# Optimization experiments

Hardware: AMD Instinct MI355X
Metric: run time of the kernel (lower is better)

## Reference

```python
import jax, jax.numpy as jnp
import numpy as np

B, T, IN, H = 64, 128, 1024, 2048  # batch, seq_len, input_size, hidden_size


def setup_inputs() -> dict:
    key = jax.random.key(0)
    k_x, k_wx, k_wa, k_b = jax.random.split(key, 4)
    x = jax.random.normal(k_x, (B, T, IN), dtype=jnp.float32)
    # stacked gate weights in torch LSTM order [i, f, g, o]; scaled like trained weights
    Wx = jax.random.normal(k_wx, (4 * H, IN), dtype=jnp.float32) * 0.05
    Wa = jax.random.normal(k_wa, (4 * H, H), dtype=jnp.float32) * 0.05
    b = jax.random.normal(k_b, (4 * H,), dtype=jnp.float32) * 0.05
    a0 = jnp.zeros((B, H), dtype=jnp.float32)
    c0 = jnp.zeros((B, H), dtype=jnp.float32)
    return {"x": x, "Wx": Wx, "Wa": Wa, "b": b, "a0": a0, "c0": c0}


def reference(x, Wx, Wa, b, a0, c0):
    # LSTM interval-propagation forward pass (the concrete forward of My_lstm):
    #   y* = W*x @ x_t + b* + W*a @ a_{t-1}
    #   c_t = sigmoid(yf) * c_{t-1} + sigmoid(yi) * tanh(yg)
    #   a_t = sigmoid(yo) * tanh(c_t)
    # a0=c0=0 reproduces the a0=None/c0=None code path exactly.
    H_ = Wa.shape[1]

    def step(carry, x_t):
        a_prev, c_prev = carry  # each [B, H]
        # one fused GEMM over all 4 gates: [B, 4H]
        y = x_t @ Wx.T + a_prev @ Wa.T + b
        yi, yf, yg, yo = jnp.split(y, 4, axis=-1)
        c_t = jax.nn.sigmoid(yf) * c_prev + jax.nn.sigmoid(yi) * jnp.tanh(yg)
        a_t = jax.nn.sigmoid(yo) * jnp.tanh(c_t)
        return (a_t, c_t), (a_t, c_t, yi, yf, yg, yo)

    xs = jnp.swapaxes(x, 0, 1)  # [T, B, IN] for scan over time
    _, (a, c, yi, yf, yg, yo) = jax.lax.scan(step, (a0, c0), xs)
    # back to [B, T, H] as in the torch module
    to_bt = lambda z: jnp.swapaxes(z, 0, 1)
    return (to_bt(a), to_bt(c), to_bt(yi), to_bt(yf), to_bt(yg), to_bt(yo))
```

## Files before the change

### kernel.cpp

```cpp
#include <hip/hip_runtime.h>
#include <hip/hip_bf16.h>

#define B_   64
#define T_   128
#define IN_  1024
#define H_   2048
#define H4_  8192
#define BT_  8192
#define BTH_ 16777216LL

typedef __attribute__((ext_vector_type(8))) short short8;
typedef __attribute__((ext_vector_type(4))) float f32x4;

__device__ __forceinline__ unsigned short f32_to_bf16_rne(float f) {
    union { float f; unsigned int u; } v; v.f = f;
    return (unsigned short)((v.u + 0x7fffu + ((v.u >> 16) & 1u)) >> 16);
}

__device__ __forceinline__ void gload_lds16(const unsigned short* g, unsigned short* l) {
    __builtin_amdgcn_global_load_lds(
        (const __attribute__((address_space(1))) unsigned int*)g,
        (__attribute__((address_space(3))) unsigned int*)l,
        16, 0, 0);
}

__global__ void cvt_bf16_kernel(const float* __restrict__ src,
                                unsigned short* __restrict__ dst, long n) {
    long i = ((long)blockIdx.x * blockDim.x + threadIdx.x) * 4;
    long stride = (long)gridDim.x * blockDim.x * 4;
    for (; i < n; i += stride) {
        float4 v = *reinterpret_cast<const float4*>(src + i);
        ushort4 o;
        o.x = f32_to_bf16_rne(v.x);
        o.y = f32_to_bf16_rne(v.y);
        o.z = f32_to_bf16_rne(v.z);
        o.w = f32_to_bf16_rne(v.w);
        *reinterpret_cast<ushort4*>(dst + i) = o;
    }
}

__global__ void copy_f32_kernel(const float* __restrict__ src,
                                float* __restrict__ dst, long n) {
    long i = ((long)blockIdx.x * blockDim.x + threadIdx.x) * 4;
    long stride = (long)gridDim.x * blockDim.x * 4;
    for (; i < n; i += stride)
        *reinterpret_cast<float4*>(dst + i) =
            *reinterpret_cast<const float4*>(src + i);
}

__global__ __launch_bounds__(256) void gemm_yx(
    const unsigned short* __restrict__ Xb,
    const unsigned short* __restrict__ Wxb,
    const float* __restrict__ bias,
    float* __restrict__ out)
{
    int bid = blockIdx.x;
    int sw  = (bid & 7) * 512 + (bid >> 3);
    int nb  = sw & 63;
    int mb  = sw >> 6;
    int m0  = mb * 128;
    int n0  = nb * 128;

    int tid  = threadIdx.x;
    int wave = tid >> 6;
    int lane = tid & 63;
    int col  = lane & 15;
    int quad = lane >> 4;
    int wm   = wave >> 1;
    int wn   = wave & 1;

    __shared__ unsigned short As[128 * 32];
    __shared__ unsigned short Bs[128 * 32];

    f32x4 acc[4][4];
#pragma unroll
    for (int i = 0; i < 4; i++)
#pragma unroll
        for (int j = 0; j < 4; j++) acc[i][j] = (f32x4){0.f, 0.f, 0.f, 0.f};

    for (int k0 = 0; k0 < IN_; k0 += 32) {
#pragma unroll
        for (int r = 0; r < 2; r++) {
            int idx = r * 256 + tid;
            int row = idx >> 2;
            int c8  = (idx & 3) * 8;
            int dbase = (r * 256 + wave * 64) * 8;
            gload_lds16(Xb  + (size_t)(m0 + row) * IN_ + k0 + c8, &As[dbase]);
            gload_lds16(Wxb + (size_t)(n0 + row) * IN_ + k0 + c8, &Bs[dbase]);
        }
        __syncthreads();

        short8 af[4], bf[4];
#pragma unroll
        for (int mt = 0; mt < 4; mt++)
            af[mt] = *(const short8*)&As[(wm * 64 + mt * 16 + col) * 32 + quad * 8];
#pragma unroll
        for (int nt = 0; nt < 4; nt++)
            bf[nt] = *(const short8*)&Bs[(wn * 64 + nt * 16 + col) * 32 + quad * 8];
#pragma unroll
        for (int mt = 0; mt < 4; mt++)
#pragma unroll
            for (int nt = 0; nt < 4; nt++)
                acc[mt][nt] = __builtin_amdgcn_mfma_f32_16x16x32_bf16(
                    af[mt], bf[nt], acc[mt][nt], 0, 0, 0);
        __syncthreads();
    }

#pragma unroll
    for (int nt = 0; nt < 4; nt++) {
        int n = n0 + wn * 64 + nt * 16 + col;
        int g = n >> 11;
        int h = n & 2047;
        float bv = bias[n];
        float* slab = out + (size_t)(2 + g) * BTH_ + h;
#pragma unroll
        for (int mt = 0; mt < 4; mt++)
#pragma unroll
            for (int r = 0; r < 4; r++) {
                int m = m0 + wm * 64 + mt * 16 + quad * 4 + r;
                slab[(size_t)m * H_] = acc[mt][nt][r] + bv;
            }
    }
}

__global__ __launch_bounds__(512) void lstm_step(
    const unsigned short* __restrict__ Wab,
    const unsigned short* __restrict__ a_prev,
    float* __restrict__ c_state,
    unsigned short* __restrict__ a_next,
    float* __restrict__ out,
    int t)
{
    int j    = blockIdx.x;
    int mh   = j & 1;
    int ht   = j >> 1;
    int h0   = ht * 16;
    int m0   = mh * 32;
    int w    = threadIdx.x >> 6;
    int g    = w & 3;
    int kh   = w >> 2;
    int lane = threadIdx.x & 63;
    int col  = lane & 15;
    int quad = lane >> 4;

    const unsigned short* brow =
        Wab + (size_t)(g * H_ + h0 + col) * H_ + kh * 1024;
    const unsigned short* arow0 =
        a_prev + (size_t)(m0 + col) * H_ + kh * 1024;
    const unsigned short* arow1 =
        a_prev + (size_t)(m0 + 16 + col) * H_ + kh * 1024;

    f32x4 acc[2];
    acc[0] = (f32x4){0.f, 0.f, 0.f, 0.f};
    acc[1] = acc[0];

#pragma unroll 4
    for (int k0 = 0; k0 < 1024; k0 += 32) {
        short8 bfrag = *(const short8*)(brow  + k0 + quad * 8);
        short8 af0   = *(const short8*)(arow0 + k0 + quad * 8);
        short8 af1   = *(const short8*)(arow1 + k0 + quad * 8);
        acc[0] = __builtin_amdgcn_mfma_f32_16x16x32_bf16(af0, bfrag, acc[0], 0, 0, 0);
        acc[1] = __builtin_amdgcn_mfma_f32_16x16x32_bf16(af1, bfrag, acc[1], 0, 0, 0);
    }

    __shared__ float yt[2][4][32][17];
#pragma unroll
    for (int mt = 0; mt < 2; mt++)
#pragma unroll
        for (int r = 0; r < 4; r++) {
            int lm = mt * 16 + quad * 4 + r;
            yt[kh][g][lm][col] = acc[mt][r];
        }
    __syncthreads();

    int f  = threadIdx.x;
    int lm = f >> 4;
    int hl = f & 15;
    int b  = m0 + lm;
    int h  = h0 + hl;
    long long oidx = ((long long)b * T_ + t) * H_ + h;

    float yi = yt[0][0][lm][hl] + yt[1][0][lm][hl] + out[2 * BTH_ + oidx];
    float yf = yt[0][1][lm][hl] + yt[1][1][lm][hl] + out[3 * BTH_ + oidx];
    float yg = yt[0][2][lm][hl] + yt[1][2][lm][hl] + out[4 * BTH_ + oidx];
    float yo = yt[0][3][lm][hl] + yt[1][3][lm][hl] + out[5 * BTH_ + oidx];
    out[2 * BTH_ + oidx] = yi;
    out[3 * BTH_ + oidx] = yf;
    out[4 * BTH_ + oidx] = yg;
    out[5 * BTH_ + oidx] = yo;

    float cp = c_state[b * H_ + h];
    float si = 1.f / (1.f + __expf(-yi));
    float sf = 1.f / (1.f + __expf(-yf));
    float so = 1.f / (1.f + __expf(-yo));
    float tg = tanhf(yg);
    float ct = sf * cp + si * tg;
    float at = so * tanhf(ct);

    c_state[b * H_ + h] = ct;
    out[oidx]          = at;
    out[BTH_ + oidx]   = ct;
    a_next[b * H_ + h] = f32_to_bf16_rne(at);
}

extern "C" void kernel_launch(void* const* d_in, const int* in_sizes, int n_in,
                              void* d_out, int out_size, void* d_ws, size_t ws_size,
                              hipStream_t stream) {
    const float* x    = (const float*)d_in[0];
    const float* Wx   = (const float*)d_in[1];
    const float* Wa   = (const float*)d_in[2];
    const float* bias = (const float*)d_in[3];
    const float* a0   = (const float*)d_in[4];
    const float* c0   = (const float*)d_in[5];
    float* out = (float*)d_out;

    unsigned short* xb    = (unsigned short*)d_ws;
    unsigned short* wxb   = xb  + (size_t)BT_ * IN_;
    unsigned short* wab   = wxb + (size_t)H4_ * IN_;
    unsigned short* abuf0 = wab + (size_t)H4_ * H_;
    unsigned short* abuf1 = abuf0 + (size_t)B_ * H_;
    float*          cst   = (float*)(abuf1 + (size_t)B_ * H_);

    cvt_bf16_kernel<<<2048, 256, 0, stream>>>(x,  xb,  (long)BT_ * IN_);
    cvt_bf16_kernel<<<2048, 256, 0, stream>>>(Wx, wxb, (long)H4_ * IN_);
    cvt_bf16_kernel<<<2048, 256, 0, stream>>>(Wa, wab, (long)H4_ * H_);
    cvt_bf16_kernel<<<128,  256, 0, stream>>>(a0, abuf0, (long)B_ * H_);
    copy_f32_kernel<<<128,  256, 0, stream>>>(c0, cst,   (long)B_ * H_);

    gemm_yx<<<(BT_ / 128) * (H4_ / 128), 256, 0, stream>>>(xb, wxb, bias, out);

    for (int t = 0; t < T_; ++t) {
        const unsigned short* ap = (t & 1) ? abuf1 : abuf0;
        unsigned short*       an = (t & 1) ? abuf0 : abuf1;
        lstm_step<<<256, 512, 0, stream>>>(wab, ap, cst, an, out, t);
    }
}
```

Baseline: 3.964 ms.

## Replace per-timestep LSTM launches with persistent cooperative kernel holding weights in registers

The 128 per-timestep kernel launches are replaced by a single cooperative persistent kernel. It loads each block's slice of the recurrent weights into registers once, keeps the cell state in a register, and separates timesteps with grid.sync. This removes per-step launch overhead and the repeated weight reloads from global memory, at the cost of heavy register pressure and a grid-wide barrier every step. The input-projection GEMM also gains an XOR swizzle on its LDS layout to reduce bank conflicts.

Measured after the change: 15.44 ms. 3.9x slower.

```diff
diff --git a/kernel.cpp b/kernel.cpp
--- a/kernel.cpp
+++ b/kernel.cpp
@@ -1,5 +1,8 @@
 #include <hip/hip_runtime.h>
 #include <hip/hip_bf16.h>
+#include <hip/hip_cooperative_groups.h>
+
+namespace cg = cooperative_groups;
 
 #define B_   64
 #define T_   128
@@ -39,15 +42,6 @@
     }
 }
 
-__global__ void copy_f32_kernel(const float* __restrict__ src,
-                                float* __restrict__ dst, long n) {
-    long i = ((long)blockIdx.x * blockDim.x + threadIdx.x) * 4;
-    long stride = (long)gridDim.x * blockDim.x * 4;
-    for (; i < n; i += stride)
-        *reinterpret_cast<float4*>(dst + i) =
-            *reinterpret_cast<const float4*>(src + i);
-}
-
 __global__ __launch_bounds__(256) void gemm_yx(
     const unsigned short* __restrict__ Xb,
     const unsigned short* __restrict__ Wxb,
@@ -83,20 +77,25 @@
         for (int r = 0; r < 2; r++) {
             int idx = r * 256 + tid;
             int row = idx >> 2;
-            int c8  = (idx & 3) * 8;
+            int u   = idx & 3;
+            int ug  = u ^ ((row >> 1) & 3);
             int dbase = (r * 256 + wave * 64) * 8;
-            gload_lds16(Xb  + (size_t)(m0 + row) * IN_ + k0 + c8, &As[dbase]);
-            gload_lds16(Wxb + (size_t)(n0 + row) * IN_ + k0 + c8, &Bs[dbase]);
+            gload_lds16(Xb  + (size_t)(m0 + row) * IN_ + k0 + ug * 8, &As[dbase]);
+            gload_lds16(Wxb + (size_t)(n0 + row) * IN_ + k0 + ug * 8, &Bs[dbase]);
         }
         __syncthreads();
 
         short8 af[4], bf[4];
 #pragma unroll
-        for (int mt = 0; mt < 4; mt++)
-            af[mt] = *(const short8*)&As[(wm * 64 + mt * 16 + col) * 32 + quad * 8];
-#pragma unroll
-        for (int nt = 0; nt < 4; nt++)
-            bf[nt] = *(const short8*)&Bs[(wn * 64 + nt * 16 + col) * 32 + quad * 8];
+        for (int mt = 0; mt < 4; mt++) {
+            int ra = wm * 64 + mt * 16 + col;
+            af[mt] = *(const short8*)&As[ra * 32 + (quad ^ ((ra >> 1) & 3)) * 8];
+        }
+#pragma unroll
+        for (int nt = 0; nt < 4; nt++) {
+            int rb = wn * 64 + nt * 16 + col;
+            bf[nt] = *(const short8*)&Bs[rb * 32 + (quad ^ ((rb >> 1) & 3)) * 8];
+        }
 #pragma unroll
         for (int mt = 0; mt < 4; mt++)
 #pragma unroll
@@ -123,84 +122,91 @@
     }
 }
 
-__global__ __launch_bounds__(512) void lstm_step(
+__global__ __launch_bounds__(512) void lstm_persistent(
     const unsigned short* __restrict__ Wab,
-    const unsigned short* __restrict__ a_prev,
-    float* __restrict__ c_state,
-    unsigned short* __restrict__ a_next,
-    float* __restrict__ out,
-    int t)
+    unsigned short* __restrict__ abuf0,
+    unsigned short* __restrict__ abuf1,
+    const float* __restrict__ c0,
+    float* __restrict__ out)
 {
-    int j    = blockIdx.x;
-    int mh   = j & 1;
-    int ht   = j >> 1;
-    int h0   = ht * 16;
-    int m0   = mh * 32;
-    int w    = threadIdx.x >> 6;
-    int g    = w & 3;
-    int kh   = w >> 2;
-    int lane = threadIdx.x & 63;
-    int col  = lane & 15;
-    int quad = lane >> 4;
-
-    const unsigned short* brow =
-        Wab + (size_t)(g * H_ + h0 + col) * H_ + kh * 1024;
-    const unsigned short* arow0 =
-        a_prev + (size_t)(m0 + col) * H_ + kh * 1024;
-    const unsigned short* arow1 =
-        a_prev + (size_t)(m0 + 16 + col) * H_ + kh * 1024;
-
-    f32x4 acc[2];
-    acc[0] = (f32x4){0.f, 0.f, 0.f, 0.f};
-    acc[1] = acc[0];
-
-#pragma unroll 4
-    for (int k0 = 0; k0 < 1024; k0 += 32) {
-        short8 bfrag = *(const short8*)(brow  + k0 + quad * 8);
-        short8 af0   = *(const short8*)(arow0 + k0 + quad * 8);
-        short8 af1   = *(const short8*)(arow1 + k0 + quad * 8);
-        acc[0] = __builtin_amdgcn_mfma_f32_16x16x32_bf16(af0, bfrag, acc[0], 0, 0, 0);
-        acc[1] = __builtin_amdgcn_mfma_f32_16x16x32_bf16(af1, bfrag, acc[1], 0, 0, 0);
-    }
-
-    __shared__ float yt[2][4][32][17];
-#pragma unroll
-    for (int mt = 0; mt < 2; mt++)
-#pragma unroll
-        for (int r = 0; r < 4; r++) {
-            int lm = mt * 16 + quad * 4 + r;
-            yt[kh][g][lm][col] = acc[mt][r];
-        }
-    __syncthreads();
-
-    int f  = threadIdx.x;
-    int lm = f >> 4;
-    int hl = f & 15;
-    int b  = m0 + lm;
-    int h  = h0 + hl;
-    long long oidx = ((long long)b * T_ + t) * H_ + h;
-
-    float yi = yt[0][0][lm][hl] + yt[1][0][lm][hl] + out[2 * BTH_ + oidx];
-    float yf = yt[0][1][lm][hl] + yt[1][1][lm][hl] + out[3 * BTH_ + oidx];
-    float yg = yt[0][2][lm][hl] + yt[1][2][lm][hl] + out[4 * BTH_ + oidx];
-    float yo = yt[0][3][lm][hl] + yt[1][3][lm][hl] + out[5 * BTH_ + oidx];
-    out[2 * BTH_ + oidx] = yi;
-    out[3 * BTH_ + oidx] = yf;
-    out[4 * BTH_ + oidx] = yg;
-    out[5 * BTH_ + oidx] = yo;
-
-    float cp = c_state[b * H_ + h];
-    float si = 1.f / (1.f + __expf(-yi));
-    float sf = 1.f / (1.f + __expf(-yf));
-    float so = 1.f / (1.f + __expf(-yo));
-    float tg = tanhf(yg);
-    float ct = sf * cp + si * tg;
-    float at = so * tanhf(ct);
-
-    c_state[b * H_ + h] = ct;
-    out[oidx]          = at;
-    out[BTH_ + oidx]   = ct;
-    a_next[b * H_ + h] = f32_to_bf16_rne(at);
+    cg::grid_group grid = cg::this_grid();
+
+    int blk  = blockIdx.x;
+    int h0   = blk * 8;
+    int tid  = threadIdx.x;
+    int w    = tid >> 6;
+    int kh   = w >> 1;
+    int gp   = w & 1;
+    int lane = tid & 63;
+    int c    = lane & 15;
+    int q    = lane >> 4;
+
+    int gate = gp * 2 + (c >> 3);
+    const unsigned short* wrow =
+        Wab + (size_t)(gate * H_ + h0 + (c & 7)) * H_ + kh * 512 + q * 8;
+    short8 wreg[16];
+#pragma unroll
+    for (int kq = 0; kq < 16; kq++)
+        wreg[kq] = *(const short8*)(wrow + kq * 32);
+
+    int bb = tid >> 3;
+    int hl = tid & 7;
+    float c_reg = c0[bb * H_ + h0 + hl];
+
+    __shared__ float yt[4][2][64][17];
+
+    for (int t = 0; t < T_; ++t) {
+        const unsigned short* ap = (t & 1) ? abuf1 : abuf0;
+        unsigned short*       an = (t & 1) ? abuf0 : abuf1;
+
+        const unsigned short* ab = ap + (size_t)c * H_ + kh * 512 + q * 8;
+        f32x4 acc[4];
+#pragma unroll
+        for (int mt = 0; mt < 4; mt++) acc[mt] = (f32x4){0.f, 0.f, 0.f, 0.f};
+
+#pragma unroll
+        for (int kq = 0; kq < 16; kq++) {
+#pragma unroll
+            for (int mt = 0; mt < 4; mt++) {
+                short8 af = *(const short8*)(ab + (size_t)mt * 16 * H_ + kq * 32);
+                acc[mt] = __builtin_amdgcn_mfma_f32_16x16x32_bf16(
+                    af, wreg[kq], acc[mt], 0, 0, 0);
+            }
+        }
+
+#pragma unroll
+        for (int mt = 0; mt < 4; mt++)
+#pragma unroll
+            for (int r = 0; r < 4; r++)
+                yt[kh][gp][mt * 16 + q * 4 + r][c] = acc[mt][r];
+        __syncthreads();
+
+        long long oidx = ((long long)bb * T_ + t) * H_ + h0 + hl;
+        float y[4];
+#pragma unroll
+        for (int g2 = 0; g2 < 4; g2++) {
+            int cc  = (g2 & 1) * 8 + hl;
+            int gpp = g2 >> 1;
+            float v = yt[0][gpp][bb][cc] + yt[1][gpp][bb][cc] +
+                      yt[2][gpp][bb][cc] + yt[3][gpp][bb][cc];
+            v += out[(size_t)(2 + g2) * BTH_ + oidx];
+            out[(size_t)(2 + g2) * BTH_ + oidx] = v;
+            y[g2] = v;
+        }
+        float si = 1.f / (1.f + __expf(-y[0]));
+        float sf = 1.f / (1.f + __expf(-y[1]));
+        float so = 1.f / (1.f + __expf(-y[3]));
+        float tg = tanhf(y[2]);
+        c_reg = sf * c_reg + si * tg;
+        float at = so * tanhf(c_reg);
+
+        out[oidx]         = at;
+        out[BTH_ + oidx]  = c_reg;
+        an[bb * H_ + h0 + hl] = f32_to_bf16_rne(at);
+
+        __threadfence();
+        grid.sync();
+    }
 }
 
 extern "C" void kernel_launch(void* const* d_in, const int* in_sizes, int n_in,
@@ -219,19 +225,22 @@
     unsigned short* wab   = wxb + (size_t)H4_ * IN_;
     unsigned short* abuf0 = wab + (size_t)H4_ * H_;
     unsigned short* abuf1 = abuf0 + (size_t)B_ * H_;
-    float*          cst   = (float*)(abuf1 + (size_t)B_ * H_);
 
     cvt_bf16_kernel<<<2048, 256, 0, stream>>>(x,  xb,  (long)BT_ * IN_);
     cvt_bf16_kernel<<<2048, 256, 0, stream>>>(Wx, wxb, (long)H4_ * IN_);
     cvt_bf16_kernel<<<2048, 256, 0, stream>>>(Wa, wab, (long)H4_ * H_);
     cvt_bf16_kernel<<<128,  256, 0, stream>>>(a0, abuf0, (long)B_ * H_);
-    copy_f32_kernel<<<128,  256, 0, stream>>>(c0, cst,   (long)B_ * H_);
 
     gemm_yx<<<(BT_ / 128) * (H4_ / 128), 256, 0, stream>>>(xb, wxb, bias, out);
 
-    for (int t = 0; t < T_; ++t) {
-        const unsigned short* ap = (t & 1) ? abuf1 : abuf0;
-        unsigned short*       an = (t & 1) ? abuf0 : abuf1;
-        lstm_step<<<256, 512, 0, stream>>>(wab, ap, cst, an, out, t);
-    }
-}
+    const unsigned short* wab_c = wab;
+    const float* c0_c = c0;
+    void* kargs[5];
+    kargs[0] = (void*)&wab_c;
+    kargs[1] = (void*)&abuf0;
+    kargs[2] = (void*)&abuf1;
+    kargs[3] = (void*)&c0_c;
+    kargs[4] = (void*)&out;
+    hipLaunchCooperativeKernel((const void*)lstm_persistent,
+                               dim3(256), dim3(512), kargs, 0, stream);
+}
```
